# Kernel tuning notes

Hardware: AMD Instinct MI355X
Metric: run time of the kernel (lower is better)

The kernel has to match this reference:

```python
import jax, jax.numpy as jnp
import numpy as np

HEADS = 4
DIM_HEAD = 32
SCALE = DIM_HEAD ** -0.5


def setup_inputs() -> dict:
    key = jax.random.key(0)
    k1, k2, k3 = jax.random.split(key, 3)
    b, c, h, w = 4, 128, 64, 64
    hidden = HEADS * DIM_HEAD  # 128
    x = jax.random.normal(k1, (b, c, h, w), dtype=jnp.float32)
    w_qkv = jax.random.normal(k2, (3 * hidden, c), dtype=jnp.float32) * 0.02  # 1x1 conv, no bias
    w_out = jax.random.normal(k3, (c, hidden), dtype=jnp.float32) * 0.02      # 1x1 conv
    b_out = jnp.zeros((c,), dtype=jnp.float32)
    return {"x": x, "w_qkv": w_qkv, "w_out": w_out, "b_out": b_out}


def reference(x, w_qkv, w_out, b_out):
    b, c, h, w = x.shape
    n = h * w
    hidden = HEADS * DIM_HEAD
    # 1x1 conv == channel matmul: [3*hidden, c] x [b, c, h, w] -> [b, 3*hidden, h, w]
    qkv = jnp.einsum('oc,bchw->bohw', w_qkv, x)
    q, k, v = jnp.split(qkv, 3, axis=1)
    # b (heads dh) h w -> b heads dh (h w)
    def to_tokens(t):
        return t.reshape(b, HEADS, DIM_HEAD, n)
    q, k, v = to_tokens(q) * SCALE, to_tokens(k), to_tokens(v)
    sim = jnp.einsum('bhdi,bhdj->bhij', q, k)          # [b, heads, n, n]
    attn = jax.nn.softmax(sim, axis=-1)                 # max-subtract is folded in (detached amax)
    out = jnp.einsum('bhij,bhdj->bhid', attn, v)        # [b, heads, n, dh]
    # b h n d -> b (h d) H W
    out = out.transpose(0, 1, 3, 2).reshape(b, hidden, h, w)
    return jnp.einsum('oc,bchw->bohw', w_out, out) + b_out[None, :, None, None]
```

## Files before the change

kernel.cpp:

```cpp
#include <hip/hip_runtime.h>

typedef float f32x4 __attribute__((ext_vector_type(4)));
typedef short s16x8 __attribute__((ext_vector_type(8)));
typedef unsigned int u32;
typedef unsigned int u32x4 __attribute__((ext_vector_type(4)));

#define SCALE 0.17677669529663687f
#define LOG2E 1.4426950408889634f

__device__ __forceinline__ unsigned short f2bf(float f) {
    unsigned u = __builtin_bit_cast(unsigned, f);
    u += 0x7fffu + ((u >> 16) & 1u);
    return (unsigned short)(u >> 16);
}

__device__ __forceinline__ float fexp2(float x) {
#if __has_builtin(__builtin_amdgcn_exp2f)
    return __builtin_amdgcn_exp2f(x);
#else
    return exp2f(x);
#endif
}

__device__ __forceinline__ u32 cvtpk(float lo, float hi) {
    u32 r;
    asm("v_cvt_pk_bf16_f32 %0, %1, %2" : "=v"(r) : "v"(lo), "v"(hi));
    return r;
}

#define MFMA16(a, b, c) __builtin_amdgcn_mfma_f32_16x16x32_bf16((a), (b), (c), 0, 0, 0)

__global__ __launch_bounds__(256) void k_qkv(const float* __restrict__ x,
                                             const float* __restrict__ w,
                                             unsigned short* __restrict__ Qb,
                                             unsigned short* __restrict__ Kb,
                                             unsigned short* __restrict__ Vf) {
    __shared__ unsigned short ldsT[64 * 136];
    const int tid = threadIdx.x;
    const int t0 = blockIdx.x * 64;
    const int o0 = blockIdx.y * 64;
    const int b = t0 >> 12;
    const int s0 = t0 & 4095;

    {
        const int t = tid & 63;
        const int cg = (tid >> 6) * 32;
        const float* xp = x + ((size_t)b * 128 + cg) * 4096 + s0 + t;
#pragma unroll
        for (int i = 0; i < 32; ++i)
            ldsT[t * 136 + cg + i] = f2bf(xp[(size_t)i * 4096]);
    }
    __syncthreads();

    const int lane = tid & 63;
    const int wv = tid >> 6;
    const int ln = lane & 15, lg = lane >> 4;
    const int ow = o0 + wv * 16;

    s16x8 aW[4];
#pragma unroll
    for (int ks = 0; ks < 4; ++ks) {
        const float* wp = w + (size_t)(ow + ln) * 128 + ks * 32 + lg * 8;
        s16x8 a;
#pragma unroll
        for (int j = 0; j < 8; ++j) a[j] = (short)f2bf(wp[j]);
        aW[ks] = a;
    }

    f32x4 acc[4] = {{0, 0, 0, 0}, {0, 0, 0, 0}, {0, 0, 0, 0}, {0, 0, 0, 0}};
#pragma unroll
    for (int ts = 0; ts < 4; ++ts) {
#pragma unroll
        for (int ks = 0; ks < 4; ++ks) {
            s16x8 bx = *(const s16x8*)&ldsT[(ts * 16 + ln) * 136 + ks * 32 + lg * 8];
            acc[ts] = MFMA16(aW[ks], bx, acc[ts]);
        }
    }

#pragma unroll
    for (int ts = 0; ts < 4; ++ts) {
        const int s = s0 + ts * 16 + ln;
#pragma unroll
        for (int r = 0; r < 4; ++r) {
            const int o = ow + lg * 4 + r;
            const float v = acc[ts][r];
            if (o < 128) {
                const int h = o >> 5, d = o & 31;
                Qb[((size_t)(b * 4 + h) * 4096 + s) * 32 + d] = f2bf(v * (SCALE * LOG2E));
            } else if (o < 256) {
                const int oo = o - 128, h = oo >> 5, d = oo & 31;
                const int js = s & 31, g = js >> 3, r4 = js & 7;
                const int slot = (r4 < 4) ? (g * 4 + r4) : (16 + g * 4 + (r4 - 4));
                const int sp = (s & ~31) | slot;
                Kb[((size_t)(b * 4 + h) * 4096 + sp) * 32 + d] = f2bf(v);
            } else {
                const int oo = o - 256, h = oo >> 5, d = oo & 31;
                const int bh = b * 4 + h;
                const int jb = s >> 5, js = s & 31;
                const int lanep = (js >> 3) * 16 + (d & 15);
                const size_t idx = ((((size_t)bh * 128 + jb) * 2 + (d >> 4)) * 64 + lanep) * 8 + (js & 7);
                Vf[idx] = f2bf(v);
            }
        }
    }
}

__global__ __launch_bounds__(512) void k_attn(const unsigned short* __restrict__ Qb,
                                              const unsigned short* __restrict__ Kb,
                                              const unsigned short* __restrict__ Vf,
                                              unsigned short* __restrict__ att) {
    __shared__ float comb[4][64][18];
    const int tid = threadIdx.x;
    const int lane = tid & 63;
    const int wv = tid >> 6;
    const int ln = lane & 15, lg = lane >> 4;
    const int bh = blockIdx.y;
    const int i0 = blockIdx.x * 128 + (wv & 3) * 32;
    const int khalf = wv >> 2;
    const size_t base = (size_t)bh * 4096 * 32;

    const s16x8 bQ0 = *(const s16x8*)(Qb + base + (size_t)(i0 + ln) * 32 + lg * 8);
    const s16x8 bQ1 = *(const s16x8*)(Qb + base + (size_t)(i0 + 16 + ln) * 32 + lg * 8);

    const int j0 = khalf * 2048;
    const unsigned short* kp = Kb + base + (size_t)(j0 + ln) * 32 + lg * 8;
    const unsigned short* vp = Vf + (size_t)bh * 131072 + (size_t)(khalf * 64) * 1024 + lane * 8;

    const f32x4 zf = {0.f, 0.f, 0.f, 0.f};
    f32x4 acc00 = zf, acc01 = zf, acc10 = zf, acc11 = zf;
    float lsum0 = 0.f, lsum1 = 0.f;

    s16x8 K0 = *(const s16x8*)(kp);
    s16x8 K1 = *(const s16x8*)(kp + 16 * 32);
    s16x8 V0 = *(const s16x8*)(vp);
    s16x8 V1 = *(const s16x8*)(vp + 512);

    auto body = [&](s16x8 cK0, s16x8 cK1, s16x8 cV0, s16x8 cV1) {
        const f32x4 S00 = MFMA16(cK0, bQ0, zf);
        const f32x4 S01 = MFMA16(cK1, bQ0, zf);
        const f32x4 S10 = MFMA16(cK0, bQ1, zf);
        const f32x4 S11 = MFMA16(cK1, bQ1, zf);
        float p00[4], p01[4], p10[4], p11[4];
#pragma unroll
        for (int r = 0; r < 4; ++r) {
            p00[r] = fexp2(S00[r]);
            p01[r] = fexp2(S01[r]);
            p10[r] = fexp2(S10[r]);
            p11[r] = fexp2(S11[r]);
        }
        lsum0 += ((p00[0] + p00[1]) + (p00[2] + p00[3])) + ((p01[0] + p01[1]) + (p01[2] + p01[3]));
        lsum1 += ((p10[0] + p10[1]) + (p10[2] + p10[3])) + ((p11[0] + p11[1]) + (p11[2] + p11[3]));
        u32x4 a0, a1;
        a0.x = cvtpk(p00[0], p00[1]);
        a0.y = cvtpk(p00[2], p00[3]);
        a0.z = cvtpk(p01[0], p01[1]);
        a0.w = cvtpk(p01[2], p01[3]);
        a1.x = cvtpk(p10[0], p10[1]);
        a1.y = cvtpk(p10[2], p10[3]);
        a1.z = cvtpk(p11[0], p11[1]);
        a1.w = cvtpk(p11[2], p11[3]);
        const s16x8 aP0 = __builtin_bit_cast(s16x8, a0);
        const s16x8 aP1 = __builtin_bit_cast(s16x8, a1);
        acc00 = MFMA16(aP0, cV0, acc00);
        acc01 = MFMA16(aP0, cV1, acc01);
        acc10 = MFMA16(aP1, cV0, acc10);
        acc11 = MFMA16(aP1, cV1, acc11);
    };

    for (int it = 0; it < 63; ++it) {
        kp += 32 * 32;
        vp += 1024;
        s16x8 nK0 = *(const s16x8*)(kp);
        s16x8 nK1 = *(const s16x8*)(kp + 16 * 32);
        s16x8 nV0 = *(const s16x8*)(vp);
        s16x8 nV1 = *(const s16x8*)(vp + 512);
        body(K0, K1, V0, V1);
        K0 = nK0; K1 = nK1; V0 = nV0; V1 = nV1;
    }
    body(K0, K1, V0, V1);

    if (wv >= 4) {
        float* p = &comb[wv - 4][lane][0];
        p[0] = acc00[0]; p[1] = acc00[1]; p[2] = acc00[2]; p[3] = acc00[3];
        p[4] = acc01[0]; p[5] = acc01[1]; p[6] = acc01[2]; p[7] = acc01[3];
        p[8] = lsum0;
        p[9] = acc10[0]; p[10] = acc10[1]; p[11] = acc10[2]; p[12] = acc10[3];
        p[13] = acc11[0]; p[14] = acc11[1]; p[15] = acc11[2]; p[16] = acc11[3];
        p[17] = lsum1;
    }
    __syncthreads();
    if (wv < 4) {
        const float* p = &comb[wv][lane][0];
        acc00[0] += p[0]; acc00[1] += p[1]; acc00[2] += p[2]; acc00[3] += p[3];
        acc01[0] += p[4]; acc01[1] += p[5]; acc01[2] += p[6]; acc01[3] += p[7];
        lsum0 += p[8];
        acc10[0] += p[9]; acc10[1] += p[10]; acc10[2] += p[11]; acc10[3] += p[12];
        acc11[0] += p[13]; acc11[1] += p[14]; acc11[2] += p[15]; acc11[3] += p[16];
        lsum1 += p[17];
        lsum0 += __shfl_xor(lsum0, 16);
        lsum0 += __shfl_xor(lsum0, 32);
        lsum1 += __shfl_xor(lsum1, 16);
        lsum1 += __shfl_xor(lsum1, 32);
        const int b = bh >> 2, h = bh & 3;
#pragma unroll
        for (int r = 0; r < 4; ++r) {
            const float rs0 = __shfl(lsum0, 4 * lg + r);
            const float rs1 = __shfl(lsum1, 4 * lg + r);
            const float ri0 = 1.0f / rs0;
            const float ri1 = 1.0f / rs1;
            const int q0 = i0 + lg * 4 + r;
            const int q1 = i0 + 16 + lg * 4 + r;
            const size_t off0 = ((size_t)b * 4096 + q0) * 128 + h * 32;
            const size_t off1 = ((size_t)b * 4096 + q1) * 128 + h * 32;
            att[off0 + ln] = f2bf(acc00[r] * ri0);
            att[off0 + 16 + ln] = f2bf(acc01[r] * ri0);
            att[off1 + ln] = f2bf(acc10[r] * ri1);
            att[off1 + 16 + ln] = f2bf(acc11[r] * ri1);
        }
    }
}

__global__ __launch_bounds__(256) void k_out(const unsigned short* __restrict__ att,
                                             const float* __restrict__ w,
                                             const float* __restrict__ bias,
                                             float* __restrict__ out) {
    const int tid = threadIdx.x;
    const int lane = tid & 63;
    const int wv = tid >> 6;
    const int ln = lane & 15, lg = lane >> 4;
    const int t0 = blockIdx.x * 64;
    const int o0 = blockIdx.y * 64;
    const int ow = o0 + wv * 16;
    const int b = t0 >> 12, s0 = t0 & 4095;

    s16x8 aW[4];
#pragma unroll
    for (int ks = 0; ks < 4; ++ks) {
        const float* wp = w + (size_t)(ow + ln) * 128 + ks * 32 + lg * 8;
        s16x8 a;
#pragma unroll
        for (int j = 0; j < 8; ++j) a[j] = (short)f2bf(wp[j]);
        aW[ks] = a;
    }

    f32x4 acc[4] = {{0, 0, 0, 0}, {0, 0, 0, 0}, {0, 0, 0, 0}, {0, 0, 0, 0}};
#pragma unroll
    for (int ts = 0; ts < 4; ++ts) {
#pragma unroll
        for (int ks = 0; ks < 4; ++ks) {
            s16x8 bx = *(const s16x8*)(att + ((size_t)t0 + ts * 16 + ln) * 128 + ks * 32 + lg * 8);
            acc[ts] = MFMA16(aW[ks], bx, acc[ts]);
        }
    }

#pragma unroll
    for (int ts = 0; ts < 4; ++ts) {
        const int s = s0 + ts * 16 + ln;
#pragma unroll
        for (int r = 0; r < 4; ++r) {
            const int o = ow + lg * 4 + r;
            out[((size_t)b * 128 + o) * 4096 + s] = acc[ts][r] + bias[o];
        }
    }
}

extern "C" void kernel_launch(void* const* d_in, const int* in_sizes, int n_in,
                              void* d_out, int out_size, void* d_ws, size_t ws_size,
                              hipStream_t stream) {
    const float* x = (const float*)d_in[0];
    const float* w_qkv = (const float*)d_in[1];
    const float* w_out = (const float*)d_in[2];
    const float* b_out = (const float*)d_in[3];
    float* out = (float*)d_out;

    unsigned short* Qb = (unsigned short*)d_ws;
    unsigned short* Kb = Qb + (size_t)16 * 4096 * 32;
    unsigned short* Vf = Kb + (size_t)16 * 4096 * 32;
    unsigned short* att = Vf + (size_t)16 * 4096 * 32;

    k_qkv<<<dim3(256, 6), 256, 0, stream>>>(x, w_qkv, Qb, Kb, Vf);
    k_attn<<<dim3(32, 16), 512, 0, stream>>>(Qb, Kb, Vf, att);
    k_out<<<dim3(256, 2), 256, 0, stream>>>(att, w_out, b_out, out);
}
```

Baseline: 78.99 us.

## Stage K/V tiles in shared memory with double buffering across all waves

Each block now handles 256 queries. All 8 waves sweep the full key range and share K/V tiles that are cooperatively loaded into double-buffered LDS, in place of each wave streaming K/V from global memory with a split-K and an LDS combine. This is meant to cut redundant global K/V traffic and remove the final cross-wave reduction. The cost is a block barrier every 128 keys, LDS read traffic, and only 256 blocks in the grid, which may underfill the 256 CUs and reduce latency hiding.

```diff
diff --git a/kernel.cpp b/kernel.cpp
--- a/kernel.cpp
+++ b/kernel.cpp
@@ -109,31 +109,24 @@
                                               const unsigned short* __restrict__ Kb,
                                               const unsigned short* __restrict__ Vf,
                                               unsigned short* __restrict__ att) {
-    __shared__ float comb[4][64][18];
+    __shared__ __align__(16) char lds[2][16384];
     const int tid = threadIdx.x;
     const int lane = tid & 63;
     const int wv = tid >> 6;
     const int ln = lane & 15, lg = lane >> 4;
     const int bh = blockIdx.y;
-    const int i0 = blockIdx.x * 128 + (wv & 3) * 32;
-    const int khalf = wv >> 2;
+    const int i0 = blockIdx.x * 256 + wv * 32;
     const size_t base = (size_t)bh * 4096 * 32;
 
     const s16x8 bQ0 = *(const s16x8*)(Qb + base + (size_t)(i0 + ln) * 32 + lg * 8);
     const s16x8 bQ1 = *(const s16x8*)(Qb + base + (size_t)(i0 + 16 + ln) * 32 + lg * 8);
 
-    const int j0 = khalf * 2048;
-    const unsigned short* kp = Kb + base + (size_t)(j0 + ln) * 32 + lg * 8;
-    const unsigned short* vp = Vf + (size_t)bh * 131072 + (size_t)(khalf * 64) * 1024 + lane * 8;
+    const char* gK = (const char*)Kb + base * 2;
+    const char* gV = (const char*)Vf + (size_t)bh * 262144;
 
     const f32x4 zf = {0.f, 0.f, 0.f, 0.f};
     f32x4 acc00 = zf, acc01 = zf, acc10 = zf, acc11 = zf;
     float lsum0 = 0.f, lsum1 = 0.f;
-
-    s16x8 K0 = *(const s16x8*)(kp);
-    s16x8 K1 = *(const s16x8*)(kp + 16 * 32);
-    s16x8 V0 = *(const s16x8*)(vp);
-    s16x8 V1 = *(const s16x8*)(vp + 512);
 
     auto body = [&](s16x8 cK0, s16x8 cK1, s16x8 cV0, s16x8 cV1) {
         const f32x4 S00 = MFMA16(cK0, bQ0, zf);
@@ -167,56 +160,59 @@
         acc11 = MFMA16(aP1, cV1, acc11);
     };
 
-    for (int it = 0; it < 63; ++it) {
-        kp += 32 * 32;
-        vp += 1024;
-        s16x8 nK0 = *(const s16x8*)(kp);
-        s16x8 nK1 = *(const s16x8*)(kp + 16 * 32);
-        s16x8 nV0 = *(const s16x8*)(vp);
-        s16x8 nV1 = *(const s16x8*)(vp + 512);
-        body(K0, K1, V0, V1);
-        K0 = nK0; K1 = nK1; V0 = nV0; V1 = nV1;
-    }
-    body(K0, K1, V0, V1);
-
-    if (wv >= 4) {
-        float* p = &comb[wv - 4][lane][0];
-        p[0] = acc00[0]; p[1] = acc00[1]; p[2] = acc00[2]; p[3] = acc00[3];
-        p[4] = acc01[0]; p[5] = acc01[1]; p[6] = acc01[2]; p[7] = acc01[3];
-        p[8] = lsum0;
-        p[9] = acc10[0]; p[10] = acc10[1]; p[11] = acc10[2]; p[12] = acc10[3];
-        p[13] = acc11[0]; p[14] = acc11[1]; p[15] = acc11[2]; p[16] = acc11[3];
-        p[17] = lsum1;
-    }
+    auto COMPUTE = [&](int buf) {
+        const char* kb = lds[buf];
+        const char* vb = lds[buf] + 8192;
+#pragma unroll
+        for (int ii = 0; ii < 4; ++ii) {
+            const s16x8 cK0 = *(const s16x8*)(kb + ii * 2048 + ln * 64 + lg * 16);
+            const s16x8 cK1 = *(const s16x8*)(kb + ii * 2048 + 1024 + ln * 64 + lg * 16);
+            const s16x8 cV0 = *(const s16x8*)(vb + ii * 2048 + lane * 16);
+            const s16x8 cV1 = *(const s16x8*)(vb + ii * 2048 + 1024 + lane * 16);
+            body(cK0, cK1, cV0, cV1);
+        }
+    };
+
+    s16x8 kr = *(const s16x8*)(gK + tid * 16);
+    s16x8 vr = *(const s16x8*)(gV + tid * 16);
+    *(s16x8*)(lds[0] + tid * 16) = kr;
+    *(s16x8*)(lds[0] + 8192 + tid * 16) = vr;
     __syncthreads();
-    if (wv < 4) {
-        const float* p = &comb[wv][lane][0];
-        acc00[0] += p[0]; acc00[1] += p[1]; acc00[2] += p[2]; acc00[3] += p[3];
-        acc01[0] += p[4]; acc01[1] += p[5]; acc01[2] += p[6]; acc01[3] += p[7];
-        lsum0 += p[8];
-        acc10[0] += p[9]; acc10[1] += p[10]; acc10[2] += p[11]; acc10[3] += p[12];
-        acc11[0] += p[13]; acc11[1] += p[14]; acc11[2] += p[15]; acc11[3] += p[16];
-        lsum1 += p[17];
-        lsum0 += __shfl_xor(lsum0, 16);
-        lsum0 += __shfl_xor(lsum0, 32);
-        lsum1 += __shfl_xor(lsum1, 16);
-        lsum1 += __shfl_xor(lsum1, 32);
-        const int b = bh >> 2, h = bh & 3;
-#pragma unroll
-        for (int r = 0; r < 4; ++r) {
-            const float rs0 = __shfl(lsum0, 4 * lg + r);
-            const float rs1 = __shfl(lsum1, 4 * lg + r);
-            const float ri0 = 1.0f / rs0;
-            const float ri1 = 1.0f / rs1;
-            const int q0 = i0 + lg * 4 + r;
-            const int q1 = i0 + 16 + lg * 4 + r;
-            const size_t off0 = ((size_t)b * 4096 + q0) * 128 + h * 32;
-            const size_t off1 = ((size_t)b * 4096 + q1) * 128 + h * 32;
-            att[off0 + ln] = f2bf(acc00[r] * ri0);
-            att[off0 + 16 + ln] = f2bf(acc01[r] * ri0);
-            att[off1 + ln] = f2bf(acc10[r] * ri1);
-            att[off1 + 16 + ln] = f2bf(acc11[r] * ri1);
-        }
+    kr = *(const s16x8*)(gK + 8192 + tid * 16);
+    vr = *(const s16x8*)(gV + 8192 + tid * 16);
+
+    for (int t = 0; t < 32; ++t) {
+        COMPUTE(t & 1);
+        if (t < 31) {
+            *(s16x8*)(lds[(t + 1) & 1] + tid * 16) = kr;
+            *(s16x8*)(lds[(t + 1) & 1] + 8192 + tid * 16) = vr;
+            if (t < 30) {
+                kr = *(const s16x8*)(gK + (size_t)(t + 2) * 8192 + tid * 16);
+                vr = *(const s16x8*)(gV + (size_t)(t + 2) * 8192 + tid * 16);
+            }
+        }
+        __syncthreads();
+    }
+
+    lsum0 += __shfl_xor(lsum0, 16);
+    lsum0 += __shfl_xor(lsum0, 32);
+    lsum1 += __shfl_xor(lsum1, 16);
+    lsum1 += __shfl_xor(lsum1, 32);
+    const int b = bh >> 2, h = bh & 3;
+#pragma unroll
+    for (int r = 0; r < 4; ++r) {
+        const float rs0 = __shfl(lsum0, 4 * lg + r);
+        const float rs1 = __shfl(lsum1, 4 * lg + r);
+        const float ri0 = 1.0f / rs0;
+        const float ri1 = 1.0f / rs1;
+        const int q0 = i0 + lg * 4 + r;
+        const int q1 = i0 + 16 + lg * 4 + r;
+        const size_t off0 = ((size_t)b * 4096 + q0) * 128 + h * 32;
+        const size_t off1 = ((size_t)b * 4096 + q1) * 128 + h * 32;
+        att[off0 + ln] = f2bf(acc00[r] * ri0);
+        att[off0 + 16 + ln] = f2bf(acc01[r] * ri0);
+        att[off1 + ln] = f2bf(acc10[r] * ri1);
+        att[off1 + 16 + ln] = f2bf(acc11[r] * ri1);
     }
 }
 
@@ -279,6 +275,6 @@
     unsigned short* att = Vf + (size_t)16 * 4096 * 32;
 
     k_qkv<<<dim3(256, 6), 256, 0, stream>>>(x, w_qkv, Qb, Kb, Vf);
-    k_attn<<<dim3(32, 16), 512, 0, stream>>>(Qb, Kb, Vf, att);
+    k_attn<<<dim3(16, 16), 512, 0, stream>>>(Qb, Kb, Vf, att);
     k_out<<<dim3(256, 2), 256, 0, stream>>>(att, w_out, b_out, out);
 }
```

Result: faster. 76.29 us (-3.4%).
